# Kernel optimization log

Measured on AMD Instinct MI355X. Metric: run time of the kernel, lower is better.

Reference implementation:

```python
import jax, jax.numpy as jnp
import numpy as np

TEMPERATURE = 1.0
EPS = 1e-8
B, D, N, K = 2048, 32, 8192, 30


def setup_inputs() -> dict:
    key = jax.random.key(0)
    k1, k2, k3 = jax.random.split(key, 3)
    z_current = jax.random.normal(k1, (B, D), dtype=jnp.float32)
    pre_knn_indices = jax.random.randint(k2, (N, K), 0, N, dtype=jnp.int64 if jax.config.jax_enable_x64 else jnp.int32)
    sample_indices = jax.random.randint(k3, (B,), 0, N, dtype=jnp.int64 if jax.config.jax_enable_x64 else jnp.int32)
    return {"z_current": z_current, "pre_knn_indices": pre_knn_indices, "sample_indices": sample_indices}


def reference(z_current, pre_knn_indices, sample_indices):
    b = z_current.shape[0]
    eye = jnp.eye(b, dtype=bool)
    # pairwise Euclidean distance via gram trick: (B,B), avoids (B,B,D) intermediate
    sq = jnp.sum(z_current * z_current, axis=-1)
    d2 = jnp.maximum(sq[:, None] + sq[None, :] - 2.0 * (z_current @ z_current.T), 0.0)
    d2_safe = jnp.where(eye, 1.0, d2)  # avoid sqrt(0) on diagonal (masked below anyway)
    dist = jnp.sqrt(d2_safe)
    sim = jnp.where(eye, -jnp.inf, -dist / TEMPERATURE)
    soft_neighbors = jax.nn.softmax(sim, axis=1)  # (B,B)
    # neighbor mask: j is kept iff global id of j is in pre-kNN set of i, and j != i
    knn = pre_knn_indices[sample_indices]  # (B,K) global ids of i's pre-neighbors
    in_set = (knn[:, :, None] == sample_indices[None, None, :]).any(axis=1)  # (B,B)
    mask = in_set & ~eye
    s = jnp.sum(soft_neighbors * mask, axis=1)  # (B,)
    valid = mask.any(axis=1)
    count = valid.sum()
    loss_i = -jnp.log(s + EPS)
    total = jnp.sum(jnp.where(valid, loss_i, 0.0))
    return jnp.where(count > 0, total / count, jnp.float32(0.0))
```

## Files before the change

### kernel.cpp

```cpp
#include <hip/hip_runtime.h>
#include <math.h>

#define Bsz 2048
#define Ddim 32
#define Nsz 8192
#define Kk 30

__global__ __launch_bounds__(256) void softnp_mask(
    const float* __restrict__ z,
    const int*   __restrict__ pre_knn,
    const int*   __restrict__ samp,
    unsigned*    __restrict__ M,
    float*       __restrict__ sq)
{
    __shared__ unsigned bits[32 * (Nsz / 32)];
    const int t  = threadIdx.x;
    const int wc = blockIdx.x >> 2;
    const int js = (blockIdx.x & 3) * 512;

    uint4* b4 = (uint4*)bits;
    #pragma unroll
    for (int c = 0; c < 8; ++c) b4[t + c * 256] = make_uint4(0u, 0u, 0u, 0u);
    __syncthreads();

    for (int v = t; v < 32 * Kk; v += 256) {
        const int r  = v / Kk, k = v - r * Kk;
        const int id = pre_knn[(size_t)samp[wc * 32 + r] * Kk + k];
        atomicOr(&bits[r * (Nsz / 32) + (id >> 5)], 1u << (id & 31));
    }
    __syncthreads();

    #pragma unroll
    for (int c = 0; c < 2; ++c) {
        const int j  = js + t + c * 256;
        const int sj = samp[j];
        const int w  = sj >> 5, bsh = sj & 31;
        unsigned word = 0u;
        #pragma unroll
        for (int r = 0; r < 32; ++r)
            word |= ((bits[r * (Nsz / 32) + w] >> bsh) & 1u) << r;
        M[(size_t)j * 64 + wc] = word;
        if (wc == 0) {
            float s = 0.f;
            const float4* zj = (const float4*)(z + (size_t)j * Ddim);
            #pragma unroll
            for (int d = 0; d < 8; ++d) {
                const float4 a = zj[d];
                s += a.x * a.x + a.y * a.y + a.z * a.z + a.w * a.w;
            }
            sq[j] = s;
        }
    }
}

__global__ __launch_bounds__(256) void softnp_den(
    const float* __restrict__ z,
    const unsigned* __restrict__ M,
    const float* __restrict__ sq,
    float*       __restrict__ wsden,
    float*       __restrict__ wsnum)
{
    const int t  = threadIdx.x;
    const int it = blockIdx.x >> 7;
    const int s  = blockIdx.x & 127;
    const int i0 = it * 256;
    const int j0 = s * 16;
    const int row = i0 + t;

    float4 zi[8];
    const float4* zr = (const float4*)(z + (size_t)row * Ddim);
    #pragma unroll
    for (int d = 0; d < 8; ++d) zi[d] = zr[d];
    float si2 = 0.f;
    #pragma unroll
    for (int d = 0; d < 8; ++d)
        si2 += zi[d].x * zi[d].x + zi[d].y * zi[d].y
             + zi[d].z * zi[d].z + zi[d].w * zi[d].w;

    unsigned mw[16];
    #pragma unroll
    for (int c = 0; c < 16; ++c)
        mw[c] = M[(size_t)(j0 + c) * 64 + ((unsigned)row >> 5)];
    const int bsh = row & 31;

    float den = 0.f, num = 0.f;
    #pragma unroll
    for (int c = 0; c < 16; ++c) {
        const int jg = j0 + c;
        const float* zj = z + (size_t)jg * Ddim;
        float dot = 0.f;
        #pragma unroll
        for (int d = 0; d < Ddim; ++d) dot += zj[d] * (((const float*)zi)[d]);
        const float d2 = fmaxf(si2 + sq[jg] - 2.f * dot, 0.f);
        const float e  = (jg == row) ? 0.f : __expf(-sqrtf(d2));
        den += e;
        num += ((mw[c] >> bsh) & 1u) ? e : 0.f;
    }

    wsden[(size_t)s * Bsz + row] = den;
    wsnum[(size_t)s * Bsz + row] = num;
}

__global__ __launch_bounds__(256) void softnp_final1(
    const float* __restrict__ wsden,
    const float* __restrict__ wsnum,
    float*       __restrict__ wsf)
{
    __shared__ float rl[4], rc[4];
    const int t = threadIdx.x;
    const int r = blockIdx.x * 256 + t;
    float D = 0.f, Nm = 0.f;
    #pragma unroll 8
    for (int s = 0; s < 128; ++s) {
        D  += wsden[(size_t)s * Bsz + r];
        Nm += wsnum[(size_t)s * Bsz + r];
    }
    float loss = 0.f, cnt = 0.f;
    if (Nm > 0.f) {
        loss = -__logf(Nm / D + 1e-8f);
        cnt  = 1.f;
    }
    #pragma unroll
    for (int off = 32; off > 0; off >>= 1) {
        loss += __shfl_xor(loss, off, 64);
        cnt  += __shfl_xor(cnt,  off, 64);
    }
    const int lane = t & 63, wv = t >> 6;
    if (lane == 0) { rl[wv] = loss; rc[wv] = cnt; }
    __syncthreads();
    if (t == 0) {
        wsf[blockIdx.x]     = rl[0] + rl[1] + rl[2] + rl[3];
        wsf[8 + blockIdx.x] = rc[0] + rc[1] + rc[2] + rc[3];
    }
}

__global__ void softnp_final2(const float* __restrict__ wsf,
                              float* __restrict__ out)
{
    const int t = threadIdx.x;
    float l = (t < 8) ? wsf[t]     : 0.f;
    float c = (t < 8) ? wsf[8 + t] : 0.f;
    #pragma unroll
    for (int off = 4; off > 0; off >>= 1) {
        l += __shfl_xor(l, off, 64);
        c += __shfl_xor(c, off, 64);
    }
    if (t == 0) out[0] = (c > 0.f) ? l / c : 0.f;
}

extern "C" void kernel_launch(void* const* d_in, const int* in_sizes, int n_in,
                              void* d_out, int out_size, void* d_ws, size_t ws_size,
                              hipStream_t stream)
{
    const float* z       = (const float*)d_in[0];
    const int*   pre_knn = (const int*)d_in[1];
    const int*   samp    = (const int*)d_in[2];
    float*       out     = (float*)d_out;

    unsigned* M     = (unsigned*)d_ws;
    float*    sq    = (float*)(M + (size_t)Bsz * 64);
    float*    wsden = sq + Bsz;
    float*    wsnum = wsden + (size_t)128 * Bsz;
    float*    wsf   = wsnum + (size_t)128 * Bsz;

    softnp_mask  <<<dim3(256),  dim3(256), 0, stream>>>(z, pre_knn, samp, M, sq);
    softnp_den   <<<dim3(1024), dim3(256), 0, stream>>>(z, M, sq, wsden, wsnum);
    softnp_final1<<<dim3(8),    dim3(256), 0, stream>>>(wsden, wsnum, wsf);
    softnp_final2<<<dim3(1),    dim3(64),  0, stream>>>(wsf, out);
}
```

Measured before the change: 92.24 us.

## Fuse mask, distance and reduction into one kernel with last-block finalize

Replaces the four-kernel pipeline with a single kernel. Each thread now checks neighbor membership directly by comparing the column's sample id against its row's 30 preloaded kNN ids, which removes the bitmask build and the transposed mask matrix. Column tiles of z and their squared norms are staged in shared memory. Partial sums are combined with global atomics, and the last block, found through an atomic counter, computes the final loss. This cuts launches and workspace traffic, but adds 30 compare ops per pair, atomic contention, and a memset launch.

```diff
diff --git a/kernel.cpp b/kernel.cpp
--- a/kernel.cpp
+++ b/kernel.cpp
@@ -5,147 +5,116 @@
 #define Ddim 32
 #define Nsz 8192
 #define Kk 30
+#define TPB 256
+#define RG (Bsz / TPB)
+#define JS 64
+#define JT (Bsz / JS)
 
-__global__ __launch_bounds__(256) void softnp_mask(
+__global__ __launch_bounds__(TPB, 2) void softnp_main(
     const float* __restrict__ z,
     const int*   __restrict__ pre_knn,
     const int*   __restrict__ samp,
-    unsigned*    __restrict__ M,
-    float*       __restrict__ sq)
+    float*       __restrict__ gden,
+    float*       __restrict__ gnum,
+    unsigned*    __restrict__ ctr,
+    float*       __restrict__ out)
 {
-    __shared__ unsigned bits[32 * (Nsz / 32)];
-    const int t  = threadIdx.x;
-    const int wc = blockIdx.x >> 2;
-    const int js = (blockIdx.x & 3) * 512;
+    __shared__ float    zjt[JT * Ddim];
+    __shared__ float    sqj[JT];
+    __shared__ int      sjs[JT];
+    __shared__ float    rl[4], rc[4];
+    __shared__ unsigned amlast;
 
-    uint4* b4 = (uint4*)bits;
-    #pragma unroll
-    for (int c = 0; c < 8; ++c) b4[t + c * 256] = make_uint4(0u, 0u, 0u, 0u);
-    __syncthreads();
-
-    for (int v = t; v < 32 * Kk; v += 256) {
-        const int r  = v / Kk, k = v - r * Kk;
-        const int id = pre_knn[(size_t)samp[wc * 32 + r] * Kk + k];
-        atomicOr(&bits[r * (Nsz / 32) + (id >> 5)], 1u << (id & 31));
-    }
-    __syncthreads();
-
-    #pragma unroll
-    for (int c = 0; c < 2; ++c) {
-        const int j  = js + t + c * 256;
-        const int sj = samp[j];
-        const int w  = sj >> 5, bsh = sj & 31;
-        unsigned word = 0u;
-        #pragma unroll
-        for (int r = 0; r < 32; ++r)
-            word |= ((bits[r * (Nsz / 32) + w] >> bsh) & 1u) << r;
-        M[(size_t)j * 64 + wc] = word;
-        if (wc == 0) {
-            float s = 0.f;
-            const float4* zj = (const float4*)(z + (size_t)j * Ddim);
-            #pragma unroll
-            for (int d = 0; d < 8; ++d) {
-                const float4 a = zj[d];
-                s += a.x * a.x + a.y * a.y + a.z * a.z + a.w * a.w;
-            }
-            sq[j] = s;
-        }
-    }
-}
-
-__global__ __launch_bounds__(256) void softnp_den(
-    const float* __restrict__ z,
-    const unsigned* __restrict__ M,
-    const float* __restrict__ sq,
-    float*       __restrict__ wsden,
-    float*       __restrict__ wsnum)
-{
-    const int t  = threadIdx.x;
-    const int it = blockIdx.x >> 7;
-    const int s  = blockIdx.x & 127;
-    const int i0 = it * 256;
-    const int j0 = s * 16;
-    const int row = i0 + t;
+    const int t   = threadIdx.x;
+    const int rg  = blockIdx.x >> 6;
+    const int js  = blockIdx.x & (JS - 1);
+    const int row = rg * TPB + t;
+    const int j0  = js * JT;
 
     float4 zi[8];
     const float4* zr = (const float4*)(z + (size_t)row * Ddim);
     #pragma unroll
     for (int d = 0; d < 8; ++d) zi[d] = zr[d];
+    const int sr = samp[row];
+    int ids[Kk];
+    const int* ib = pre_knn + (size_t)sr * Kk;
+    #pragma unroll
+    for (int k = 0; k < Kk; ++k) ids[k] = ib[k];
+
     float si2 = 0.f;
     #pragma unroll
     for (int d = 0; d < 8; ++d)
         si2 += zi[d].x * zi[d].x + zi[d].y * zi[d].y
              + zi[d].z * zi[d].z + zi[d].w * zi[d].w;
 
-    unsigned mw[16];
-    #pragma unroll
-    for (int c = 0; c < 16; ++c)
-        mw[c] = M[(size_t)(j0 + c) * 64 + ((unsigned)row >> 5)];
-    const int bsh = row & 31;
+    ((float4*)zjt)[t] = ((const float4*)z)[(size_t)j0 * 8 + t];
+    if (t < JT) sjs[t] = samp[j0 + t];
+    __syncthreads();
+    if (t < JT) {
+        const float4* a = (const float4*)(zjt + t * Ddim);
+        float s = 0.f;
+        #pragma unroll
+        for (int d = 0; d < 8; ++d)
+            s += a[d].x * a[d].x + a[d].y * a[d].y
+               + a[d].z * a[d].z + a[d].w * a[d].w;
+        sqj[t] = s;
+    }
+    __syncthreads();
 
     float den = 0.f, num = 0.f;
-    #pragma unroll
-    for (int c = 0; c < 16; ++c) {
-        const int jg = j0 + c;
-        const float* zj = z + (size_t)jg * Ddim;
+    for (int c = 0; c < JT; ++c) {
+        const float4* v4 = (const float4*)(zjt + c * Ddim);
         float dot = 0.f;
         #pragma unroll
-        for (int d = 0; d < Ddim; ++d) dot += zj[d] * (((const float*)zi)[d]);
-        const float d2 = fmaxf(si2 + sq[jg] - 2.f * dot, 0.f);
-        const float e  = (jg == row) ? 0.f : __expf(-sqrtf(d2));
+        for (int d = 0; d < 8; ++d) {
+            const float4 v = v4[d];
+            dot += zi[d].x * v.x + zi[d].y * v.y + zi[d].z * v.z + zi[d].w * v.w;
+        }
+        const float d2 = fmaxf(si2 + sqj[c] - 2.f * dot, 0.f);
+        const float e  = (j0 + c == row) ? 0.f : __expf(-sqrtf(d2));
         den += e;
-        num += ((mw[c] >> bsh) & 1u) ? e : 0.f;
+        const unsigned sj = (unsigned)sjs[c];
+        unsigned mn = 0xFFFFFFFFu;
+        #pragma unroll
+        for (int k = 0; k < Kk; ++k) mn = min(mn, sj ^ (unsigned)ids[k]);
+        num += (mn == 0u) ? e : 0.f;
     }
 
-    wsden[(size_t)s * Bsz + row] = den;
-    wsnum[(size_t)s * Bsz + row] = num;
-}
+    atomicAdd(&gden[row], den);
+    atomicAdd(&gnum[row], num);
 
-__global__ __launch_bounds__(256) void softnp_final1(
-    const float* __restrict__ wsden,
-    const float* __restrict__ wsnum,
-    float*       __restrict__ wsf)
-{
-    __shared__ float rl[4], rc[4];
-    const int t = threadIdx.x;
-    const int r = blockIdx.x * 256 + t;
-    float D = 0.f, Nm = 0.f;
-    #pragma unroll 8
-    for (int s = 0; s < 128; ++s) {
-        D  += wsden[(size_t)s * Bsz + r];
-        Nm += wsnum[(size_t)s * Bsz + r];
+    __threadfence();
+    __syncthreads();
+    if (t == 0)
+        amlast = (atomicAdd(ctr, 1u) == (unsigned)gridDim.x - 1u) ? 1u : 0u;
+    __syncthreads();
+    if (amlast) {
+        __threadfence();
+        float loss = 0.f, cnt = 0.f;
+        #pragma unroll
+        for (int c = 0; c < RG; ++c) {
+            const int r = c * TPB + t;
+            const float D  = atomicAdd(&gden[r], 0.0f);
+            const float Nm = atomicAdd(&gnum[r], 0.0f);
+            if (Nm > 0.f) {
+                loss -= __logf(Nm / D + 1e-8f);
+                cnt  += 1.f;
+            }
+        }
+        #pragma unroll
+        for (int off = 32; off > 0; off >>= 1) {
+            loss += __shfl_xor(loss, off, 64);
+            cnt  += __shfl_xor(cnt,  off, 64);
+        }
+        const int lane = t & 63, wv = t >> 6;
+        if (lane == 0) { rl[wv] = loss; rc[wv] = cnt; }
+        __syncthreads();
+        if (t == 0) {
+            const float L = rl[0] + rl[1] + rl[2] + rl[3];
+            const float C = rc[0] + rc[1] + rc[2] + rc[3];
+            out[0] = (C > 0.f) ? L / C : 0.f;
+        }
     }
-    float loss = 0.f, cnt = 0.f;
-    if (Nm > 0.f) {
-        loss = -__logf(Nm / D + 1e-8f);
-        cnt  = 1.f;
-    }
-    #pragma unroll
-    for (int off = 32; off > 0; off >>= 1) {
-        loss += __shfl_xor(loss, off, 64);
-        cnt  += __shfl_xor(cnt,  off, 64);
-    }
-    const int lane = t & 63, wv = t >> 6;
-    if (lane == 0) { rl[wv] = loss; rc[wv] = cnt; }
-    __syncthreads();
-    if (t == 0) {
-        wsf[blockIdx.x]     = rl[0] + rl[1] + rl[2] + rl[3];
-        wsf[8 + blockIdx.x] = rc[0] + rc[1] + rc[2] + rc[3];
-    }
-}
-
-__global__ void softnp_final2(const float* __restrict__ wsf,
-                              float* __restrict__ out)
-{
-    const int t = threadIdx.x;
-    float l = (t < 8) ? wsf[t]     : 0.f;
-    float c = (t < 8) ? wsf[8 + t] : 0.f;
-    #pragma unroll
-    for (int off = 4; off > 0; off >>= 1) {
-        l += __shfl_xor(l, off, 64);
-        c += __shfl_xor(c, off, 64);
-    }
-    if (t == 0) out[0] = (c > 0.f) ? l / c : 0.f;
 }
 
 extern "C" void kernel_launch(void* const* d_in, const int* in_sizes, int n_in,
@@ -157,14 +126,13 @@
     const int*   samp    = (const int*)d_in[2];
     float*       out     = (float*)d_out;
 
-    unsigned* M     = (unsigned*)d_ws;
-    float*    sq    = (float*)(M + (size_t)Bsz * 64);
-    float*    wsden = sq + Bsz;
-    float*    wsnum = wsden + (size_t)128 * Bsz;
-    float*    wsf   = wsnum + (size_t)128 * Bsz;
+    float*    gden = (float*)d_ws;
+    float*    gnum = gden + Bsz;
+    unsigned* ctr  = (unsigned*)(gnum + Bsz);
 
-    softnp_mask  <<<dim3(256),  dim3(256), 0, stream>>>(z, pre_knn, samp, M, sq);
-    softnp_den   <<<dim3(1024), dim3(256), 0, stream>>>(z, M, sq, wsden, wsnum);
-    softnp_final1<<<dim3(8),    dim3(256), 0, stream>>>(wsden, wsnum, wsf);
-    softnp_final2<<<dim3(1),    dim3(64),  0, stream>>>(wsf, out);
+    hipMemsetAsync(d_ws, 0, (size_t)(2 * Bsz) * sizeof(float) + sizeof(unsigned),
+                   stream);
+
+    softnp_main<<<dim3(RG * JS), dim3(TPB), 0, stream>>>(
+        z, pre_knn, samp, gden, gnum, ctr, out);
 }
```

Result: slower. 106.1 us (+15.0%).
